# Optimization experiments

Hardware: AMD Instinct MI355X
Metric: run time of the kernel (lower is better)

## Reference

```python
import jax, jax.numpy as jnp
import numpy as np

B, Nq, C = 1, 40000, 256
Hh, L, P = 8, 4, 8
hd = C // Hh
LEVEL_SHAPES = [(128, 128), (64, 64), (32, 32), (16, 16)]


def setup_inputs() -> dict:
    key = jax.random.key(0)
    ks = jax.random.split(key, 16)
    inp = {}
    inp['query'] = jax.random.normal(ks[0], (B, Nq, C), jnp.float32)
    # reference points in [-1, 1] normalized coords (x, y)
    inp['reference_points'] = jax.random.uniform(ks[1], (B, Nq, L, 2), jnp.float32) * 2.0 - 1.0
    for i, (h, w) in enumerate(LEVEL_SHAPES):
        inp[f'feat{i}'] = jax.random.normal(ks[2 + i], (B, C, h, w), jnp.float32)
    # learned params (torch Linear y = x @ W + b, W stored as [in, out])
    inp['W_off'] = jax.random.normal(ks[6], (C, Hh * L * P * 2), jnp.float32) * 0.02
    inp['b_off'] = jax.random.normal(ks[7], (Hh * L * P * 2,), jnp.float32) * 0.5
    inp['W_attn'] = jax.random.normal(ks[8], (C, Hh * L * P), jnp.float32) * 0.02
    inp['b_attn'] = jnp.zeros((Hh * L * P,), jnp.float32)
    inp['W_val'] = jax.random.normal(ks[9], (C, C), jnp.float32) * (1.0 / np.sqrt(C))
    inp['b_val'] = jnp.zeros((C,), jnp.float32)
    inp['W_out'] = jax.random.normal(ks[10], (C, C), jnp.float32) * (1.0 / np.sqrt(C))
    inp['b_out'] = jnp.zeros((C,), jnp.float32)
    return inp


def _deform_sample(v, coords):
    # Bilinear grid_sample, align_corners=True, zeros padding.
    # v: [B, Hh, H, W, hd]; coords: [B, Hh, S, 2] in [-1, 1] (x, y)
    _, _, H, W, _ = v.shape
    x = (coords[..., 0] + 1.0) * 0.5 * (W - 1)
    y = (coords[..., 1] + 1.0) * 0.5 * (H - 1)
    x0 = jnp.floor(x)
    y0 = jnp.floor(y)
    vflat = v.reshape(v.shape[0], v.shape[1], H * W, v.shape[4])

    def corner(xi, yi, w):
        inb = (xi >= 0) & (xi <= W - 1) & (yi >= 0) & (yi <= H - 1)
        idx = (jnp.clip(yi, 0, H - 1) * W + jnp.clip(xi, 0, W - 1)).astype(jnp.int32)
        g = jnp.take_along_axis(vflat, idx[..., None], axis=2)  # [B,Hh,S,hd]
        return g * (w * inb)[..., None]

    return (corner(x0, y0, (x0 + 1 - x) * (y0 + 1 - y))
            + corner(x0 + 1, y0, (x - x0) * (y0 + 1 - y))
            + corner(x0, y0 + 1, (x0 + 1 - x) * (y - y0))
            + corner(x0 + 1, y0 + 1, (x - x0) * (y - y0)))


def reference(query, feat0, feat1, feat2, feat3, reference_points,
              W_off, b_off, W_attn, b_attn, W_val, b_val, W_out, b_out):
    feats = [feat0, feat1, feat2, feat3]
    off = (query @ W_off + b_off).reshape(B, Nq, Hh, L, P, 2)
    w = (query @ W_attn + b_attn).reshape(B, Nq, Hh, L, P)
    w = jax.nn.softmax(w, axis=-1)  # softmax over points, per level
    # samp: [B, Nq, Hh, L, P, 2]
    samp = reference_points[:, :, None, :, None, :] + jnp.tanh(off) * 0.25

    out = jnp.zeros((B, Nq, Hh, hd), jnp.float32)
    for l, f in enumerate(feats):
        Hl, Wl = f.shape[2], f.shape[3]
        v = jnp.einsum('bchw,cd->bhwd', f, W_val) + b_val  # value proj
        v = v.reshape(B, Hl, Wl, Hh, hd).transpose(0, 3, 1, 2, 4)  # [B,Hh,H,W,hd]
        coords = samp[:, :, :, l].transpose(0, 2, 1, 3, 4).reshape(B, Hh, Nq * P, 2)
        s = _deform_sample(v, coords).reshape(B, Hh, Nq, P, hd)
        wl = w[:, :, :, l].transpose(0, 2, 1, 3)  # [B,Hh,Nq,P]
        out = out + jnp.einsum('bhnpd,bhnp->bnhd', s, wl)

    return out.reshape(B, Nq, C) @ W_out + b_out
```

## Files before the change

kernel.cpp:

```cpp
#include <hip/hip_runtime.h>
#include <hip/hip_fp16.h>
#include <math.h>

#define NQ 40000

typedef short s16x8 __attribute__((ext_vector_type(8)));
typedef float f32x4 __attribute__((ext_vector_type(4)));

static constexpr int HLa[4] = {128, 64, 32, 16};
static constexpr int HWa[4] = {16384, 4096, 1024, 256};
static constexpr int VB[4] = {0, 4194304, 5242880, 5505024};

__device__ __forceinline__ short bf16hi(float x) {
    union { float f; unsigned u; } v; v.f = x;
    unsigned r = v.u + 0x7FFFu + ((v.u >> 16) & 1u);
    return (short)(r >> 16);
}
__device__ __forceinline__ float bf16f(short s) {
    union { unsigned u; float f; } v; v.u = ((unsigned)(unsigned short)s) << 16;
    return v.f;
}
__device__ __forceinline__ float fast_tanh(float x) {
    float xc = fminf(fmaxf(x, -15.f), 15.f);
    float e = __expf(2.f * xc);
    return (e - 1.f) / (e + 1.f);
}
#define MFMA16(a, b, c) __builtin_amdgcn_mfma_f32_16x16x32_bf16(a, b, c, 0, 0, 0)

__global__ __launch_bounds__(256) void prep_w(
    const float* __restrict__ Woff, const float* __restrict__ Wattn,
    const float* __restrict__ Wout, short* __restrict__ WtH, short* __restrict__ WtL)
{
    int r = blockIdx.x, c = threadIdx.x;
    float x;
    if (r < 512)      x = Woff[c * 512 + r];
    else if (r < 768) x = Wattn[c * 256 + (r - 512)];
    else              x = Wout[c * 256 + (r - 768)];
    short hi = bf16hi(x);
    WtH[r * 256 + c] = hi;
    WtL[r * 256 + c] = bf16hi(x - bf16f(hi));
}

__global__ __launch_bounds__(256) void vproj_kernel(
    const float* __restrict__ f0, const float* __restrict__ f1,
    const float* __restrict__ f2, const float* __restrict__ f3,
    const float* __restrict__ Wv, const float* __restrict__ bv,
    __half* __restrict__ v)
{
    __shared__ float fT[256 * 16];

    int bid = blockIdx.x;
    const float* f;
    int base, HWl, hw0;
    if (bid < 1024)      { f = f0; base = VB[0]; HWl = 16384; hw0 = bid * 16; }
    else if (bid < 1280) { f = f1; base = VB[1]; HWl = 4096;  hw0 = (bid - 1024) * 16; }
    else if (bid < 1344) { f = f2; base = VB[2]; HWl = 1024;  hw0 = (bid - 1280) * 16; }
    else                 { f = f3; base = VB[3]; HWl = 256;   hw0 = (bid - 1344) * 16; }

    int t = threadIdx.x;
    for (int k = 0; k < 16; ++k) {
        int idx = k * 256 + t;
        int c = idx >> 4, j = idx & 15;
        fT[idx] = f[c * HWl + hw0 + j];
    }
    __syncthreads();

    int to4 = (t & 63) * 4;
    int hw4 = (t >> 6) * 4;

    float4 bv4 = *(const float4*)(bv + to4);
    float acc[4][4];
    #pragma unroll
    for (int i = 0; i < 4; ++i) {
        acc[i][0] = bv4.x; acc[i][1] = bv4.y; acc[i][2] = bv4.z; acc[i][3] = bv4.w;
    }

    #pragma unroll 4
    for (int c = 0; c < 256; ++c) {
        float4 w4 = *(const float4*)(Wv + c * 256 + to4);
        float4 fv = *(const float4*)(fT + c * 16 + hw4);
        float fa[4] = {fv.x, fv.y, fv.z, fv.w};
        float wa[4] = {w4.x, w4.y, w4.z, w4.w};
        #pragma unroll
        for (int i = 0; i < 4; ++i)
            #pragma unroll
            for (int j = 0; j < 4; ++j)
                acc[i][j] += fa[i] * wa[j];
    }

    int hh = to4 >> 5, dd4 = to4 & 31;
    #pragma unroll
    for (int i = 0; i < 4; ++i) {
        int hw = hw0 + hw4 + i;
        __half2 h0 = __floats2half2_rn(acc[i][0], acc[i][1]);
        __half2 h1 = __floats2half2_rn(acc[i][2], acc[i][3]);
        uint2 st = make_uint2(*(unsigned*)&h0, *(unsigned*)&h1);
        *(uint2*)(v + base + (hh * HWl + hw) * 32 + dd4) = st;
    }
}

__global__ __launch_bounds__(256, 4) void msda_hp_kernel(
    const float* __restrict__ query, const float* __restrict__ refp,
    const float* __restrict__ boff,  const float* __restrict__ battn,
    const short* __restrict__ WtH,   const short* __restrict__ WtL,
    const __half* __restrict__ v,    __half* __restrict__ preTg)
{
    __shared__ __align__(16) char lds[30720];
    __half* sWh = (__half*)(lds + 16896);
    float*  sR  = (float*)(lds + 28672);

    const int t = threadIdx.x;
    const int hp = blockIdx.x & 3;
    const int n0 = (blockIdx.x >> 2) * 64;
    const int wv = t >> 6, lane = t & 63;
    const int mrow = lane & 15, kg = lane >> 4;
    float*    offW = (float*)lds + wv * 1056;
    unsigned* sPIw = (unsigned*)(lds + 25600 + wv * 768);
    uint2*    sPWw = (uint2*)(lds + 25600 + wv * 768 + 256);

    sR[t]       = refp[n0 * 8 + t];
    sR[t + 256] = refp[n0 * 8 + t + 256];
    __syncthreads();

    f32x4 accO[8], accA[4];
    {
        f32x4 z = {0.f, 0.f, 0.f, 0.f};
        #pragma unroll
        for (int j = 0; j < 8; ++j) accO[j] = z;
        #pragma unroll
        for (int j = 0; j < 4; ++j) accA[j] = z;
    }
    {
        const float* qrow = query + (n0 + wv * 16 + mrow) * 256 + kg * 8;
        const short* offH = WtH + (hp * 128 + mrow) * 256 + kg * 8;
        const short* offLo = WtL + (hp * 128 + mrow) * 256 + kg * 8;
        const short* attH = WtH + (512 + hp * 64 + mrow) * 256 + kg * 8;
        const short* attL = WtL + (512 + hp * 64 + mrow) * 256 + kg * 8;
        #pragma unroll
        for (int kk = 0; kk < 8; ++kk) {
            float4 qa = *(const float4*)(qrow + kk * 32);
            float4 qb = *(const float4*)(qrow + kk * 32 + 4);
            float qv[8] = {qa.x, qa.y, qa.z, qa.w, qb.x, qb.y, qb.z, qb.w};
            s16x8 ah, al;
            #pragma unroll
            for (int e = 0; e < 8; ++e) {
                short hi = bf16hi(qv[e]);
                ah[e] = hi;
                al[e] = bf16hi(qv[e] - bf16f(hi));
            }
            #pragma unroll
            for (int j = 0; j < 8; ++j) {
                s16x8 bh = *(const s16x8*)(offH + j * 4096 + kk * 32);
                s16x8 bl = *(const s16x8*)(offLo + j * 4096 + kk * 32);
                accO[j] = MFMA16(ah, bh, accO[j]);
                accO[j] = MFMA16(al, bh, accO[j]);
                accO[j] = MFMA16(ah, bl, accO[j]);
            }
            #pragma unroll
            for (int ja = 0; ja < 4; ++ja) {
                s16x8 bh = *(const s16x8*)(attH + ja * 4096 + kk * 32);
                s16x8 bl = *(const s16x8*)(attL + ja * 4096 + kk * 32);
                accA[ja] = MFMA16(ah, bh, accA[ja]);
                accA[ja] = MFMA16(al, bh, accA[ja]);
                accA[ja] = MFMA16(ah, bl, accA[ja]);
            }
        }
    }
    #pragma unroll
    for (int j = 0; j < 8; ++j) {
        float bb = boff[hp * 128 + j * 16 + mrow];
        #pragma unroll
        for (int r = 0; r < 4; ++r) accO[j][r] += bb;
    }
    #pragma unroll
    for (int ja = 0; ja < 4; ++ja) {
        float bb = battn[hp * 64 + ja * 16 + mrow];
        #pragma unroll
        for (int r = 0; r < 4; ++r) accA[ja][r] += bb;
    }

    #pragma unroll
    for (int ja = 0; ja < 4; ++ja) {
        int hhL = ja >> 1;
        int l   = ((ja & 1) << 1) | (mrow >> 3);
        int p   = mrow & 7;
        #pragma unroll
        for (int r = 0; r < 4; ++r) {
            float x = accA[ja][r];
            float m = fmaxf(x, __shfl_xor(x, 1));
            m = fmaxf(m, __shfl_xor(m, 2));
            m = fmaxf(m, __shfl_xor(m, 4));
            float e = __expf(x - m);
            float s = e + __shfl_xor(e, 1);
            s += __shfl_xor(s, 2);
            s += __shfl_xor(s, 4);
            int ql = wv * 16 + kg * 4 + r;
            sWh[ql * 68 + hhL * 32 + l * 8 + p] = __float2half_rn(e / s);
        }
    }

    const int l_p = (lane >> 3) & 3;
    const int Wl_p = 128 >> l_p;
    const float scl_p = 0.5f * (float)(Wl_p - 1);
    const int sg = kg, ch2 = mrow;
    const int Wl_s = 128 >> sg;
    const int HWs = Wl_s * Wl_s;
    const int dyoMul = Wl_s * 16;
    const int VBs = (sg == 0) ? VB[0] : (sg == 1) ? VB[1] : (sg == 2) ? VB[2] : VB[3];
    const __half2* vl0 = (const __half2*)(v + VBs + (2 * hp) * HWs * 32) + ch2;
    const __half2* vl1 = (const __half2*)(v + VBs + (2 * hp + 1) * HWs * 32) + ch2;

    for (int sp = 0; sp < 2; ++sp) {
        if ((kg >> 1) == sp) {
            #pragma unroll
            for (int j = 0; j < 8; ++j)
                #pragma unroll
                for (int r = 0; r < 4; ++r)
                    offW[((kg & 1) * 4 + r) * 132 + j * 16 + mrow] = accO[j][r];
        }

        for (int c8 = 0; c8 < 8; ++c8) {
            const int chunk = sp * 8 + c8;
            const int ql = wv * 16 + chunk;
            {
                float2 ll = *(const float2*)(offW + c8 * 132 + 2 * lane);
                float lx = ll.x, ly = ll.y;
                float w  = __half2float(sWh[ql * 68 + lane]);
                float rx = sR[ql * 8 + l_p * 2], ry = sR[ql * 8 + l_p * 2 + 1];
                float cx = rx + fast_tanh(lx) * 0.25f;
                float cy = ry + fast_tanh(ly) * 0.25f;
                float xx = (cx + 1.f) * scl_p, yy = (cy + 1.f) * scl_p;
                float x0f = floorf(xx), y0f = floorf(yy);
                float fx = xx - x0f, fy = yy - y0f;
                int x0 = (int)x0f, y0 = (int)y0f;
                int xc0 = min(max(x0, 0), Wl_p - 1);
                int xc1 = min(max(x0 + 1, 0), Wl_p - 1);
                int yc0 = min(max(y0, 0), Wl_p - 1);
                int yc1 = min(max(y0 + 1, 0), Wl_p - 1);
                bool bx0 = (x0 >= 0) & (x0 < Wl_p);
                bool bx1 = (x0 + 1 >= 0) & (x0 + 1 < Wl_p);
                bool by0 = (y0 >= 0) & (y0 < Wl_p);
                bool by1 = (y0 + 1 >= 0) & (y0 + 1 < Wl_p);
                float w00 = (bx0 && by0) ? (1.f - fx) * (1.f - fy) * w : 0.f;
                float w01 = (bx1 && by0) ? fx * (1.f - fy) * w : 0.f;
                float w10 = (bx0 && by1) ? (1.f - fx) * fy * w : 0.f;
                float w11 = (bx1 && by1) ? fx * fy * w : 0.f;
                unsigned pw = (unsigned)(yc0 * Wl_p + xc0)
                            | ((unsigned)(xc1 - xc0) << 14)
                            | ((unsigned)(yc1 - yc0) << 15);
                sPIw[lane] = pw;
                __half2 hA = __floats2half2_rn(w00, w01);
                __half2 hB = __floats2half2_rn(w10, w11);
                sPWw[lane] = make_uint2(*(unsigned*)&hA, *(unsigned*)&hB);
            }

            float ax = 0.f, ay = 0.f;
            #pragma unroll
            for (int iter = 0; iter < 16; ++iter) {
                const int hhL = iter >> 3, p = iter & 7;
                const int rec = hhL * 32 + sg * 8 + p;
                unsigned pw = sPIw[rec];
                uint2 ww = sPWw[rec];
                const __half2* vl = hhL ? vl1 : vl0;
                int idx = pw & 0x3FFF;
                int dxo = ((pw >> 14) & 1) * 16;
                int dyo = ((pw >> 15) & 1) * dyoMul;
                const __half2* b00 = vl + idx * 16;
                float2 fa = __half22float2(*(__half2*)&ww.x);
                float2 fb = __half22float2(*(__half2*)&ww.y);
                float2 f00 = __half22float2(b00[0]);
                float2 f01 = __half22float2(b00[dxo]);
                float2 f10 = __half22float2(b00[dyo]);
                float2 f11 = __half22float2(b00[dxo + dyo]);
                ax += fa.x * f00.x + fa.y * f01.x + fb.x * f10.x + fb.y * f11.x;
                ay += fa.x * f00.y + fa.y * f01.y + fb.x * f10.y + fb.y * f11.y;
                if ((iter & 7) == 7) {
                    float sxv = ax + __shfl_xor(ax, 16); sxv += __shfl_xor(sxv, 32);
                    float syv = ay + __shfl_xor(ay, 16); syv += __shfl_xor(syv, 32);
                    if (sg == 0)
                        *(__half2*)(preTg + (n0 + ql) * 256 + (2 * hp + hhL) * 32 + ch2 * 2) =
                            __floats2half2_rn(sxv, syv);
                    ax = 0.f; ay = 0.f;
                }
            }
        }
    }
}

__global__ __launch_bounds__(256, 4) void outproj_kernel(
    const __half* __restrict__ preTg, const short* __restrict__ WtH,
    const short* __restrict__ WtL,    const float* __restrict__ bout,
    float* __restrict__ out)
{
    __shared__ __align__(16) char lds[16896];
    short* sQh = (short*)lds;
    short* sQl = (short*)(lds + 8448);

    const int t = threadIdx.x;
    const int n0 = blockIdx.x * 16;
    const int wv = t >> 6, lane = t & 63;
    const int mrow = lane & 15, kg = lane >> 4;

    {
        int q = t & 15, seg = t >> 4;
        const __half2* src = (const __half2*)(preTg + (n0 + q) * 256 + seg * 16);
        short* dh = sQh + q * 264 + seg * 16;
        short* dl = sQl + q * 264 + seg * 16;
        #pragma unroll
        for (int jj = 0; jj < 8; ++jj) {
            float2 f = __half22float2(src[jj]);
            short h0 = bf16hi(f.x), h1 = bf16hi(f.y);
            dh[2 * jj]     = h0;
            dh[2 * jj + 1] = h1;
            dl[2 * jj]     = bf16hi(f.x - bf16f(h0));
            dl[2 * jj + 1] = bf16hi(f.y - bf16f(h1));
        }
    }
    __syncthreads();

    f32x4 accE[4];
    f32x4 z = {0.f, 0.f, 0.f, 0.f};
    #pragma unroll
    for (int e = 0; e < 4; ++e) accE[e] = z;
    const short* outH = WtH + (768 + wv * 64 + mrow) * 256 + kg * 8;
    const short* outL = WtL + (768 + wv * 64 + mrow) * 256 + kg * 8;
    const int aoff = mrow * 264 + kg * 8;
    #pragma unroll
    for (int kk = 0; kk < 8; ++kk) {
        s16x8 ah = *(const s16x8*)(sQh + aoff + kk * 32);
        s16x8 al = *(const s16x8*)(sQl + aoff + kk * 32);
        #pragma unroll
        for (int e = 0; e < 4; ++e) {
            s16x8 bh = *(const s16x8*)(outH + e * 4096 + kk * 32);
            s16x8 bl = *(const s16x8*)(outL + e * 4096 + kk * 32);
            accE[e] = MFMA16(ah, bh, accE[e]);
            accE[e] = MFMA16(al, bh, accE[e]);
            accE[e] = MFMA16(ah, bl, accE[e]);
        }
    }
    #pragma unroll
    for (int e = 0; e < 4; ++e) {
        int col = wv * 64 + e * 16 + mrow;
        float bb = bout[col];
        #pragma unroll
        for (int r = 0; r < 4; ++r)
            out[(n0 + kg * 4 + r) * 256 + col] = accE[e][r] + bb;
    }
}

extern "C" void kernel_launch(void* const* d_in, const int* in_sizes, int n_in,
                              void* d_out, int out_size, void* d_ws, size_t ws_size,
                              hipStream_t stream) {
    const float* query = (const float*)d_in[0];
    const float* refp  = (const float*)d_in[1];
    const float* f0    = (const float*)d_in[2];
    const float* f1    = (const float*)d_in[3];
    const float* f2    = (const float*)d_in[4];
    const float* f3    = (const float*)d_in[5];
    const float* Woff  = (const float*)d_in[6];
    const float* boff  = (const float*)d_in[7];
    const float* Wattn = (const float*)d_in[8];
    const float* battn = (const float*)d_in[9];
    const float* Wval  = (const float*)d_in[10];
    const float* bval  = (const float*)d_in[11];
    const float* Wout  = (const float*)d_in[12];
    const float* bout  = (const float*)d_in[13];

    char* ws = (char*)d_ws;
    __half* v  = (__half*)ws;
    short* WtH = (short*)(ws + 11141120);
    short* WtL = (short*)(ws + 11665408);
    __half* preTg = (__half*)(ws + 12189696);
    float* outp = (float*)d_out;

    prep_w<<<1024, 256, 0, stream>>>(Woff, Wattn, Wout, WtH, WtL);
    vproj_kernel<<<1360, 256, 0, stream>>>(f0, f1, f2, f3, Wval, bval, v);
    msda_hp_kernel<<<2500, 256, 0, stream>>>(query, refp, boff, battn,
                                             WtH, WtL, v, preTg);
    outproj_kernel<<<2500, 256, 0, stream>>>(preTg, WtH, WtL, bout, outp);
}
```

Before: 536.7 us.

## Gather 4 channels per lane with 8-byte loads and packed half2 FMA

```diff
diff --git a/kernel.cpp b/kernel.cpp
--- a/kernel.cpp
+++ b/kernel.cpp
@@ -202,13 +202,15 @@
     const int l_p = (lane >> 3) & 3;
     const int Wl_p = 128 >> l_p;
     const float scl_p = 0.5f * (float)(Wl_p - 1);
-    const int sg = kg, ch2 = mrow;
+    const int sg = kg;
+    const int sub = mrow >> 3;
+    const int c4 = mrow & 7;
     const int Wl_s = 128 >> sg;
     const int HWs = Wl_s * Wl_s;
     const int dyoMul = Wl_s * 16;
     const int VBs = (sg == 0) ? VB[0] : (sg == 1) ? VB[1] : (sg == 2) ? VB[2] : VB[3];
-    const __half2* vl0 = (const __half2*)(v + VBs + (2 * hp) * HWs * 32) + ch2;
-    const __half2* vl1 = (const __half2*)(v + VBs + (2 * hp + 1) * HWs * 32) + ch2;
+    const __half2* vl0 = (const __half2*)(v + VBs + (2 * hp) * HWs * 32) + c4 * 2;
+    const __half2* vl1 = (const __half2*)(v + VBs + (2 * hp + 1) * HWs * 32) + c4 * 2;
 
     for (int sp = 0; sp < 2; ++sp) {
         if ((kg >> 1) == sp) {
@@ -254,11 +256,11 @@
                 sPWw[lane] = make_uint2(*(unsigned*)&hA, *(unsigned*)&hB);
             }
 
-            float ax = 0.f, ay = 0.f;
-            #pragma unroll
-            for (int iter = 0; iter < 16; ++iter) {
-                const int hhL = iter >> 3, p = iter & 7;
-                const int rec = hhL * 32 + sg * 8 + p;
+            float ac0 = 0.f, ac1 = 0.f, ac2 = 0.f, ac3 = 0.f;
+            #pragma unroll
+            for (int iter = 0; iter < 8; ++iter) {
+                const int hhL = iter >> 2, pp = iter & 3;
+                const int rec = hhL * 32 + sg * 8 + pp * 2 + sub;
                 unsigned pw = sPIw[rec];
                 uint2 ww = sPWw[rec];
                 const __half2* vl = hhL ? vl1 : vl0;
@@ -266,21 +268,41 @@
                 int dxo = ((pw >> 14) & 1) * 16;
                 int dyo = ((pw >> 15) & 1) * dyoMul;
                 const __half2* b00 = vl + idx * 16;
-                float2 fa = __half22float2(*(__half2*)&ww.x);
-                float2 fb = __half22float2(*(__half2*)&ww.y);
-                float2 f00 = __half22float2(b00[0]);
-                float2 f01 = __half22float2(b00[dxo]);
-                float2 f10 = __half22float2(b00[dyo]);
-                float2 f11 = __half22float2(b00[dxo + dyo]);
-                ax += fa.x * f00.x + fa.y * f01.x + fb.x * f10.x + fb.y * f11.x;
-                ay += fa.x * f00.y + fa.y * f01.y + fb.x * f10.y + fb.y * f11.y;
-                if ((iter & 7) == 7) {
-                    float sxv = ax + __shfl_xor(ax, 16); sxv += __shfl_xor(sxv, 32);
-                    float syv = ay + __shfl_xor(ay, 16); syv += __shfl_xor(syv, 32);
-                    if (sg == 0)
-                        *(__half2*)(preTg + (n0 + ql) * 256 + (2 * hp + hhL) * 32 + ch2 * 2) =
-                            __floats2half2_rn(sxv, syv);
-                    ax = 0.f; ay = 0.f;
+                uint2 g00 = *(const uint2*)(b00);
+                uint2 g01 = *(const uint2*)(b00 + dxo);
+                uint2 g10 = *(const uint2*)(b00 + dyo);
+                uint2 g11 = *(const uint2*)(b00 + dxo + dyo);
+                __half2 wA = *(__half2*)&ww.x;
+                __half2 wB = *(__half2*)&ww.y;
+                __half2 w00 = __low2half2(wA),  w01 = __high2half2(wA);
+                __half2 w10 = __low2half2(wB),  w11 = __high2half2(wB);
+                __half2 s0 = __hmul2(w00, *(__half2*)&g00.x);
+                s0 = __hfma2(w01, *(__half2*)&g01.x, s0);
+                s0 = __hfma2(w10, *(__half2*)&g10.x, s0);
+                s0 = __hfma2(w11, *(__half2*)&g11.x, s0);
+                __half2 s1 = __hmul2(w00, *(__half2*)&g00.y);
+                s1 = __hfma2(w01, *(__half2*)&g01.y, s1);
+                s1 = __hfma2(w10, *(__half2*)&g10.y, s1);
+                s1 = __hfma2(w11, *(__half2*)&g11.y, s1);
+                float2 f0 = __half22float2(s0);
+                float2 f1 = __half22float2(s1);
+                ac0 += f0.x; ac1 += f0.y; ac2 += f1.x; ac3 += f1.y;
+                if ((iter & 3) == 3) {
+                    float r0 = ac0 + __shfl_xor(ac0, 8);
+                    float r1 = ac1 + __shfl_xor(ac1, 8);
+                    float r2 = ac2 + __shfl_xor(ac2, 8);
+                    float r3 = ac3 + __shfl_xor(ac3, 8);
+                    r0 += __shfl_xor(r0, 16); r1 += __shfl_xor(r1, 16);
+                    r2 += __shfl_xor(r2, 16); r3 += __shfl_xor(r3, 16);
+                    r0 += __shfl_xor(r0, 32); r1 += __shfl_xor(r1, 32);
+                    r2 += __shfl_xor(r2, 32); r3 += __shfl_xor(r3, 32);
+                    if (sg == 0 && sub == 0) {
+                        __half2 o0 = __floats2half2_rn(r0, r1);
+                        __half2 o1 = __floats2half2_rn(r2, r3);
+                        *(uint2*)(preTg + (n0 + ql) * 256 + (2 * hp + hhL) * 32 + c4 * 4) =
+                            make_uint2(*(unsigned*)&o0, *(unsigned*)&o1);
+                    }
+                    ac0 = 0.f; ac1 = 0.f; ac2 = 0.f; ac3 = 0.f;
                 }
             }
         }
```

New measurement: 558.5 us. 1.04x slower.
